# Performance work log

Measured on AMD Instinct MI355X. Metric: run time of the kernel, lower is better.

The kernel has to match this reference:

```python
import jax, jax.numpy as jnp
import numpy as np

N_NODES = 50000
N_EDGES = 800000
D_FEAT = 128
UNITS = 256
K = 3


def setup_inputs() -> dict:
    key = jax.random.key(0)
    k1, k2, k3, k4 = jax.random.split(key, 4)
    x = jax.random.normal(k1, (N_NODES, D_FEAT), dtype=jnp.float32)
    edge_index = jax.random.randint(k2, (2, N_EDGES), 0, N_NODES, dtype=jnp.int32)
    edge_weight = jnp.ones((N_EDGES,), dtype=jnp.float32)
    # glorot-uniform kernel [(K+1)*D, UNITS], zero bias
    fan_in, fan_out = D_FEAT * (K + 1), UNITS
    limit = np.sqrt(6.0 / (fan_in + fan_out)).astype(np.float32)
    kernel = jax.random.uniform(k3, (fan_in, fan_out), minval=-limit, maxval=limit, dtype=jnp.float32)
    bias = jnp.zeros((UNITS,), dtype=jnp.float32)
    return {"x": x, "edge_index": edge_index, "edge_weight": edge_weight,
            "kernel": kernel, "bias": bias}


def reference(x, edge_index, edge_weight, kernel, bias):
    n = x.shape[0]
    row, col = edge_index[0], edge_index[1]
    # symmetric GCN normalization (renorm=False: normalize first, then self-loops w=1)
    deg = jax.ops.segment_sum(edge_weight, row, num_segments=n)
    deg_inv_sqrt = jnp.where(deg > 0, jax.lax.rsqrt(jnp.where(deg > 0, deg, 1.0)), 0.0)
    normed_w = deg_inv_sqrt[row] * edge_weight * deg_inv_sqrt[col]
    loop = jnp.arange(n, dtype=row.dtype)
    row2 = jnp.concatenate([row, loop])
    col2 = jnp.concatenate([col, loop])
    w2 = jnp.concatenate([normed_w, jnp.ones((n,), dtype=normed_w.dtype)])
    # K-hop propagation, collecting each hop
    xs = [x]
    h = x
    for _ in range(K):
        msg = h[col2] * w2[:, None]            # [E+N, D] gather + scale
        h = jax.ops.segment_sum(msg, row2, num_segments=n)  # scatter-sum
        xs.append(h)
    hcat = jnp.concatenate(xs, axis=-1)        # [N, (K+1)*D]
    out = hcat @ kernel + bias
    return jax.nn.relu(out)
```

## Files before the change

### kernel.cpp

```cpp
#include <hip/hip_runtime.h>

#define NN 50000
#define NP 50048
#define NE 800000
#define D 128
#define UNITS 256
#define KTOT 512
#define SCAN_NB 50
#define NREP 16
#define CONV_NB 6250

typedef __attribute__((ext_vector_type(8))) short short8;
typedef __attribute__((ext_vector_type(4))) float floatx4;

__device__ inline unsigned short f2b(float f) {
    unsigned u = __float_as_uint(f);
    return (unsigned short)((u + 0x7fff + ((u >> 16) & 1)) >> 16);
}
__device__ inline float2 bx2f(unsigned v) {
    float2 r;
    r.x = __uint_as_float(v << 16);
    r.y = __uint_as_float(v & 0xffff0000u);
    return r;
}

__global__ void count_kernel(const int* __restrict__ row, int* __restrict__ cnt16,
                             int* __restrict__ rank, int E) {
    int e = blockIdx.x * blockDim.x + threadIdx.x;
    if (e < E) {
        int rep = (e >> 6) & (NREP - 1);
        rank[e] = atomicAdd(&cnt16[rep * NN + row[e]], 1);
    }
}

__global__ __launch_bounds__(256) void scanA_kernel(int* __restrict__ cnt16,
                                                    int* __restrict__ row_ptr,
                                                    int* __restrict__ bsum) {
    __shared__ int s[256];
    int b = blockIdx.x, t = threadIdx.x;
    int base = b * 1024 + t * 4;
    int v[4];
    int sum = 0;
#pragma unroll
    for (int i = 0; i < 4; ++i) {
        int idx = base + i;
        int tot = 0;
        if (idx < NN) {
            int c[NREP];
            int run = 0;
#pragma unroll
            for (int r = 0; r < NREP; ++r) c[r] = cnt16[r * NN + idx];
#pragma unroll
            for (int r = 0; r < NREP; ++r) {
                cnt16[r * NN + idx] = run;
                run += c[r];
            }
            tot = run;
        }
        v[i] = tot;
        sum += tot;
    }
    s[t] = sum;
    __syncthreads();
    for (int off = 1; off < 256; off <<= 1) {
        int add = (t >= off) ? s[t - off] : 0;
        __syncthreads();
        s[t] += add;
        __syncthreads();
    }
    int run = s[t] - sum;
#pragma unroll
    for (int i = 0; i < 4; ++i) {
        int idx = base + i;
        if (idx < NN) row_ptr[idx] = run;
        run += v[i];
    }
    if (t == 255) bsum[b] = s[255];
}

__global__ void scanB_kernel(int* __restrict__ bsum, int* __restrict__ row_ptr) {
    if (threadIdx.x == 0 && blockIdx.x == 0) {
        int run = 0;
        for (int i = 0; i < SCAN_NB; ++i) {
            int v = bsum[i];
            bsum[i] = run;
            run += v;
        }
        row_ptr[NN] = run;
    }
}

__global__ __launch_bounds__(256) void scanC_kernel(int* __restrict__ row_ptr,
                                                    const int* __restrict__ bsum) {
    int b = blockIdx.x, t = threadIdx.x;
    int off = bsum[b];
    int base = b * 1024 + t * 4;
#pragma unroll
    for (int i = 0; i < 4; ++i) {
        int idx = base + i;
        if (idx < NN) row_ptr[idx] += off;
    }
}

__global__ void fill_kernel(const int* __restrict__ row, const int* __restrict__ col,
                            const float* __restrict__ w, const int* __restrict__ rank,
                            const int* __restrict__ row_ptr, const int* __restrict__ cnt16,
                            int2* __restrict__ edges, int E) {
    int e = blockIdx.x * blockDim.x + threadIdx.x;
    if (e >= E) return;
    int r = row[e];
    int rep = (e >> 6) & (NREP - 1);
    int pos = row_ptr[r] + cnt16[rep * NN + r] + rank[e];
    edges[pos] = make_int2(col[e], __float_as_int(w[e]));
}

__global__ __launch_bounds__(256) void degdis_kernel(const int* __restrict__ row_ptr,
                                                     const int2* __restrict__ edges,
                                                     float* __restrict__ dis) {
    int node = blockIdx.x * 4 + (threadIdx.x >> 6);
    int l = threadIdx.x & 63;
    if (node >= NN) return;
    int beg = row_ptr[node], end = row_ptr[node + 1];
    float s = 0.f;
    for (int e = beg + l; e < end; e += 64) s += __int_as_float(edges[e].y);
#pragma unroll
    for (int off = 32; off; off >>= 1) s += __shfl_down(s, off);
    if (l == 0) dis[node] = s > 0.f ? rsqrtf(s) : 0.f;
}

__global__ __launch_bounds__(256) void prep_kernel(const float* __restrict__ x,
                                                   unsigned* __restrict__ xb,
                                                   const float* __restrict__ W,
                                                   short* __restrict__ Wt) {
    __shared__ float tile[32][33];
    if (blockIdx.x < CONV_NB) {
        int t = blockIdx.x * 256 + threadIdx.x;
        float4 v = ((const float4*)x)[t];
        uint2 o;
        o.x = (unsigned)f2b(v.x) | ((unsigned)f2b(v.y) << 16);
        o.y = (unsigned)f2b(v.z) | ((unsigned)f2b(v.w) << 16);
        ((uint2*)xb)[t] = o;
    } else {
        int b = blockIdx.x - CONV_NB;
        int kb = (b & 15) * 32;
        int nb = (b >> 4) * 32;
        int tx = threadIdx.x & 31, ty = threadIdx.x >> 5;
        for (int i = 0; i < 32; i += 8)
            tile[ty + i][tx] = W[(size_t)(kb + ty + i) * UNITS + nb + tx];
        __syncthreads();
        for (int i = 0; i < 32; i += 8)
            Wt[(size_t)(nb + ty + i) * KTOT + kb + tx] = (short)f2b(tile[tx][ty + i]);
    }
}

__device__ inline void acc8(float* acc, uint4 v, float w) {
    float2 f0 = bx2f(v.x), f1 = bx2f(v.y), f2 = bx2f(v.z), f3 = bx2f(v.w);
    acc[0] = fmaf(w, f0.x, acc[0]); acc[1] = fmaf(w, f0.y, acc[1]);
    acc[2] = fmaf(w, f1.x, acc[2]); acc[3] = fmaf(w, f1.y, acc[3]);
    acc[4] = fmaf(w, f2.x, acc[4]); acc[5] = fmaf(w, f2.y, acc[5]);
    acc[6] = fmaf(w, f3.x, acc[6]); acc[7] = fmaf(w, f3.y, acc[7]);
}

template <bool NORM>
__global__ __launch_bounds__(256) void gather_kernel(const unsigned* __restrict__ hprev,
                                                     unsigned* __restrict__ hnext,
                                                     const int* __restrict__ row_ptr,
                                                     int2* __restrict__ edges,
                                                     const float* __restrict__ dis) {
    int node = blockIdx.x * 4 + (threadIdx.x >> 6);
    if (node >= NN) return;
    int l = threadIdx.x & 63;
    int g = l >> 4;
    int s = l & 15;
    const uint4* hp4 = (const uint4*)hprev;
    int beg = row_ptr[node], end = row_ptr[node + 1];
    float dr = NORM ? dis[node] : 1.f;

    float acc[8] = {0.f, 0.f, 0.f, 0.f, 0.f, 0.f, 0.f, 0.f};
    int2 M0 = edges[(beg + g) < end ? (beg + g) : end - 1];
    int2 M1 = edges[(beg + 4 + g) < end ? (beg + 4 + g) : end - 1];
    for (int e = beg; e < end; e += 8) {
        int i0 = e + g;
        int i1 = e + 4 + g;
        int2 E0 = M0, E1 = M1;
        int en = e + 8;
        if (en < end) {
            int j0 = en + g, j1 = en + 4 + g;
            M0 = edges[j0 < end ? j0 : end - 1];
            M1 = edges[j1 < end ? j1 : end - 1];
        }
        float w0 = __int_as_float(E0.y);
        float w1 = __int_as_float(E1.y);
        if (NORM) {
            w0 *= dr * dis[E0.x];
            w1 *= dr * dis[E1.x];
        }
        w0 = (i0 < end) ? w0 : 0.f;
        w1 = (i1 < end) ? w1 : 0.f;
        uint4 v0 = hp4[(size_t)E0.x * 16 + s];
        uint4 v1 = hp4[(size_t)E1.x * 16 + s];
        acc8(acc, v0, w0);
        acc8(acc, v1, w1);
        if (NORM && s == 0) {
            if (i0 < end) edges[i0].y = __float_as_int(w0);
            if (i1 < end) edges[i1].y = __float_as_int(w1);
        }
    }
#pragma unroll
    for (int i = 0; i < 8; ++i) {
        acc[i] += __shfl_xor(acc[i], 16);
        acc[i] += __shfl_xor(acc[i], 32);
    }
    if (g == 0) {
        uint4 sv = hp4[(size_t)node * 16 + s];
        acc8(acc, sv, 1.f);
        uint4 o;
        o.x = (unsigned)f2b(acc[0]) | ((unsigned)f2b(acc[1]) << 16);
        o.y = (unsigned)f2b(acc[2]) | ((unsigned)f2b(acc[3]) << 16);
        o.z = (unsigned)f2b(acc[4]) | ((unsigned)f2b(acc[5]) << 16);
        o.w = (unsigned)f2b(acc[6]) | ((unsigned)f2b(acc[7]) << 16);
        ((uint4*)hnext)[(size_t)node * 16 + s] = o;
    }
}

__global__ __launch_bounds__(256) void gemm_mfma(const short* __restrict__ A0,
                                                 const short* __restrict__ Wt,
                                                 const float* __restrict__ bias,
                                                 float* __restrict__ C) {
    const int t = threadIdx.x;
    const int wn = t >> 6;
    const int l = t & 63;
    const int lm = l & 15;
    const int lg = l >> 4;
    const int m0 = blockIdx.x * 64;
    const int n0 = wn * 64;

    floatx4 zero = {0.f, 0.f, 0.f, 0.f};
    floatx4 acc[4][4];
#pragma unroll
    for (int r = 0; r < 4; ++r)
#pragma unroll
        for (int c = 0; c < 4; ++c) acc[r][c] = zero;

#pragma unroll 4
    for (int ks = 0; ks < KTOT; ks += 32) {
        const short* Asrc = A0 + (size_t)(ks >> 7) * ((size_t)NP * D) + (ks & 127) + lg * 8;
        const short* Bsrc = Wt + ks + lg * 8;
        short8 af[4], bfr[4];
#pragma unroll
        for (int r = 0; r < 4; ++r)
            af[r] = *(const short8*)(Asrc + (size_t)(m0 + r * 16 + lm) * D);
#pragma unroll
        for (int c = 0; c < 4; ++c)
            bfr[c] = *(const short8*)(Bsrc + (size_t)(n0 + c * 16 + lm) * KTOT);
#pragma unroll
        for (int r = 0; r < 4; ++r)
#pragma unroll
            for (int c = 0; c < 4; ++c)
                acc[r][c] = __builtin_amdgcn_mfma_f32_16x16x32_bf16(af[r], bfr[c],
                                                                    acc[r][c], 0, 0, 0);
    }

    const int q4 = lg * 4;
#pragma unroll
    for (int r = 0; r < 4; ++r) {
#pragma unroll
        for (int i = 0; i < 4; ++i) {
            int m = m0 + r * 16 + q4 + i;
            if (m < NN) {
#pragma unroll
                for (int c = 0; c < 4; ++c) {
                    int n = n0 + c * 16 + lm;
                    float v = acc[r][c][i] + bias[n];
                    C[(size_t)m * UNITS + n] = fmaxf(v, 0.f);
                }
            }
        }
    }
}

extern "C" void kernel_launch(void* const* d_in, const int* in_sizes, int n_in,
                              void* d_out, int out_size, void* d_ws, size_t ws_size,
                              hipStream_t stream) {
    const float* x = (const float*)d_in[0];
    const int* ei = (const int*)d_in[1];
    const float* ew_in = (const float*)d_in[2];
    const float* W = (const float*)d_in[3];
    const float* bias = (const float*)d_in[4];
    float* out = (float*)d_out;

    const int* row = ei;
    const int* col = ei + NE;

    float* dis = (float*)d_ws;
    int* cnt16 = (int*)(dis + NN);
    int* rank = cnt16 + NREP * NN;
    int* bsum = rank + NE;
    int* row_ptr = bsum + 64;
    int2* edges = (int2*)(row_ptr + NN + 2);
    unsigned* xb = (unsigned*)(edges + NE) + 2;
    unsigned* h1b = xb + (size_t)NP * 64;
    unsigned* h2b = h1b + (size_t)NP * 64;
    unsigned* h3b = h2b + (size_t)NP * 64;
    short* Wt = (short*)(h3b + (size_t)NP * 64);

    hipMemsetAsync(cnt16, 0, NREP * NN * sizeof(int), stream);

    count_kernel<<<(NE + 255) / 256, 256, 0, stream>>>(row, cnt16, rank, NE);
    scanA_kernel<<<SCAN_NB, 256, 0, stream>>>(cnt16, row_ptr, bsum);
    scanB_kernel<<<1, 64, 0, stream>>>(bsum, row_ptr);
    scanC_kernel<<<SCAN_NB, 256, 0, stream>>>(row_ptr, bsum);
    fill_kernel<<<(NE + 255) / 256, 256, 0, stream>>>(row, col, ew_in, rank, row_ptr, cnt16,
                                                      edges, NE);
    degdis_kernel<<<(NN + 3) / 4, 256, 0, stream>>>(row_ptr, edges, dis);
    prep_kernel<<<CONV_NB + 128, 256, 0, stream>>>(x, xb, W, Wt);

    int gat_blocks = (NN + 3) / 4;
    gather_kernel<true><<<gat_blocks, 256, 0, stream>>>(xb, h1b, row_ptr, edges, dis);
    gather_kernel<false><<<gat_blocks, 256, 0, stream>>>(h1b, h2b, row_ptr, edges, dis);
    gather_kernel<false><<<gat_blocks, 256, 0, stream>>>(h2b, h3b, row_ptr, edges, dis);

    gemm_mfma<<<NP / 64, 256, 0, stream>>>((const short*)xb, Wt, bias, out);
}
```

Measured before the change: 342.3 us.

## Stage weight tile in LDS via global_load_lds and retile GEMM grid

The GEMM now stages a 64-column slice of the transposed weight (64x512 bf16, 64KB) into shared memory with direct global-to-LDS loads, using an XOR swizzle to avoid bank conflicts. The grid becomes 2D: each block covers 128 rows and 64 output columns, with each wave taking 32 rows. This removes repeated global reads of the weight per k-step, but A rows are now read four times, once per column block. The large LDS allocation limits occupancy to about two blocks per CU.

```diff
diff --git a/kernel.cpp b/kernel.cpp
--- a/kernel.cpp
+++ b/kernel.cpp
@@ -223,38 +223,52 @@
     }
 }
 
+#define GLDS(g, l)                                                                      \
+    __builtin_amdgcn_global_load_lds((const __attribute__((address_space(1))) void*)(g), \
+                                     (__attribute__((address_space(3))) void*)(l), 16, 0, 0)
+
 __global__ __launch_bounds__(256) void gemm_mfma(const short* __restrict__ A0,
                                                  const short* __restrict__ Wt,
                                                  const float* __restrict__ bias,
                                                  float* __restrict__ C) {
+    __shared__ short Bs[64 * KTOT];
     const int t = threadIdx.x;
-    const int wn = t >> 6;
+    const int w = t >> 6;
     const int l = t & 63;
     const int lm = l & 15;
     const int lg = l >> 4;
-    const int m0 = blockIdx.x * 64;
-    const int n0 = wn * 64;
+    const int m0 = blockIdx.x * 128;
+    const int n0 = blockIdx.y * 64;
+
+    for (int j = 0; j < 16; ++j) {
+        int n = w * 16 + j;
+        const short* src = Wt + (size_t)(n0 + n) * KTOT + ((l ^ (j & 7)) * 8);
+        GLDS(src, Bs + n * KTOT);
+    }
+    __syncthreads();
 
     floatx4 zero = {0.f, 0.f, 0.f, 0.f};
-    floatx4 acc[4][4];
-#pragma unroll
-    for (int r = 0; r < 4; ++r)
+    floatx4 acc[2][4];
+#pragma unroll
+    for (int r = 0; r < 2; ++r)
 #pragma unroll
         for (int c = 0; c < 4; ++c) acc[r][c] = zero;
 
 #pragma unroll 4
-    for (int ks = 0; ks < KTOT; ks += 32) {
-        const short* Asrc = A0 + (size_t)(ks >> 7) * ((size_t)NP * D) + (ks & 127) + lg * 8;
-        const short* Bsrc = Wt + ks + lg * 8;
-        short8 af[4], bfr[4];
-#pragma unroll
-        for (int r = 0; r < 4; ++r)
-            af[r] = *(const short8*)(Asrc + (size_t)(m0 + r * 16 + lm) * D);
-#pragma unroll
-        for (int c = 0; c < 4; ++c)
-            bfr[c] = *(const short8*)(Bsrc + (size_t)(n0 + c * 16 + lm) * KTOT);
-#pragma unroll
-        for (int r = 0; r < 4; ++r)
+    for (int j = 0; j < 16; ++j) {
+        const short* Asrc = A0 + (size_t)(j >> 2) * ((size_t)NP * D) + (j & 3) * 32 + lg * 8;
+        short8 af[2], bfr[4];
+#pragma unroll
+        for (int r = 0; r < 2; ++r)
+            af[r] = *(const short8*)(Asrc + (size_t)(m0 + w * 32 + r * 16 + lm) * D);
+        int kc = j * 4 + lg;
+#pragma unroll
+        for (int c = 0; c < 4; ++c) {
+            int n = c * 16 + lm;
+            bfr[c] = *(const short8*)&Bs[n * KTOT + ((kc ^ (n & 7)) * 8)];
+        }
+#pragma unroll
+        for (int r = 0; r < 2; ++r)
 #pragma unroll
             for (int c = 0; c < 4; ++c)
                 acc[r][c] = __builtin_amdgcn_mfma_f32_16x16x32_bf16(af[r], bfr[c],
@@ -263,10 +277,10 @@
 
     const int q4 = lg * 4;
 #pragma unroll
-    for (int r = 0; r < 4; ++r) {
+    for (int r = 0; r < 2; ++r) {
 #pragma unroll
         for (int i = 0; i < 4; ++i) {
-            int m = m0 + r * 16 + q4 + i;
+            int m = m0 + w * 32 + r * 16 + q4 + i;
             if (m < NN) {
 #pragma unroll
                 for (int c = 0; c < 4; ++c) {
@@ -320,5 +334,6 @@
     gather_kernel<false><<<gat_blocks, 256, 0, stream>>>(h1b, h2b, row_ptr, edges, dis);
     gather_kernel<false><<<gat_blocks, 256, 0, stream>>>(h2b, h3b, row_ptr, edges, dis);
 
-    gemm_mfma<<<NP / 64, 256, 0, stream>>>((const short*)xb, Wt, bias, out);
-}
+    gemm_mfma<<<dim3(NP / 128, UNITS / 64), 256, 0, stream>>>(
+        (const short*)xb, Wt, bias, out);
+}
```

Result: faster. 335.1 us (-2.1%).
